# Kernel tuning notes

Hardware: AMD Instinct MI355X
Metric: run time of the kernel (lower is better)

## Reference

```python
import jax, jax.numpy as jnp
import numpy as np

IMG_H = 448
IMG_W = 448
NEG = jnp.float32(-1e30)


def make_anchors(h, w, stride, size):
    # centers at (x*stride, y*stride), single scale, ratio 1; row-major (y, x) order
    ys = jnp.arange(h, dtype=jnp.float32) * stride
    xs = jnp.arange(w, dtype=jnp.float32) * stride
    cy, cx = jnp.meshgrid(ys, xs, indexing='ij')
    cx, cy = cx.reshape(-1), cy.reshape(-1)
    half = 0.5 * size
    return jnp.stack([cx - half, cy - half, cx + half, cy + half], axis=1)  # [h*w, 4]


def iou_one_vs_all(box, boxes):
    x1 = jnp.maximum(box[0], boxes[:, 0]); y1 = jnp.maximum(box[1], boxes[:, 1])
    x2 = jnp.minimum(box[2], boxes[:, 2]); y2 = jnp.minimum(box[3], boxes[:, 3])
    inter = jnp.maximum(x2 - x1, 0.) * jnp.maximum(y2 - y1, 0.)
    a1 = (box[2] - box[0]) * (box[3] - box[1])
    a2 = (boxes[:, 2] - boxes[:, 0]) * (boxes[:, 3] - boxes[:, 1])
    return inter / (a1 + a2 - inter)


def nms_topk(anchors, scores, valid, iou_thr, topk):
    # greedy NMS: invalid (<= mean) boxes get -inf score so they are never selected
    s0 = jnp.where(valid, scores, NEG)

    def body(k, carry):
        s, out = carry
        idx = jnp.argmax(s)
        box = anchors[idx]
        sup = iou_one_vs_all(box, anchors) > iou_thr
        s = jnp.where(sup, NEG, s).at[idx].set(NEG)
        out = out.at[k].set(box)
        return (s, out)

    _, out = jax.lax.fori_loop(0, topk, body, (s0, jnp.zeros((topk, 4), jnp.float32)))
    return out  # [topk, 4]


def get_att_roi(att, stride, size, iou_thr, topk):
    n, _, h, w = att.shape
    corner = jnp.zeros((h, w), att.dtype).at[int(0.1 * h):int(0.9 * h), int(0.1 * w):int(0.9 * w)].set(1.0)
    scores = (att[:, 0] * corner).reshape(n, -1)
    valid = scores > scores.mean(axis=1, keepdims=True)  # score threshold = per-sample mean
    anchors = make_anchors(h, w, float(stride), float(size))
    boxes = jax.vmap(lambda s, v: nms_topk(anchors, s, v, iou_thr, topk))(scores, valid)  # [n, topk, 4]
    boxes = jnp.stack([
        jnp.maximum(boxes[..., 0], 0.),
        jnp.maximum(boxes[..., 1], 0.),
        jnp.minimum(boxes[..., 2], IMG_W - 1.),
        jnp.minimum(boxes[..., 3], IMG_H - 1.),
    ], axis=-1)
    ids = jnp.broadcast_to(jnp.arange(n, dtype=jnp.float32)[:, None, None], (n, topk, 1))
    return jnp.concatenate([ids, boxes], axis=-1).reshape(n * topk, 5)


def crop_resize(xi, x1i, y1i, cw, ch):
    # bilinear resize of integer crop xi[:, y1i:y1i+ch, x1i:x1i+cw] to full (H, W),
    # align_corners=False (matches F.interpolate)
    C, H, W = xi.shape

    def axis_idx(n_out, start, clen):
        s = jnp.maximum((jnp.arange(n_out, dtype=jnp.float32) + 0.5) * (clen.astype(jnp.float32) / n_out) - 0.5, 0.)
        i0 = jnp.floor(s).astype(jnp.int32)
        i1 = jnp.minimum(i0 + 1, clen - 1)
        return start + i0, start + i1, s - i0

    gy0, gy1, fy = axis_idx(H, y1i, ch)
    gx0, gx1, fx = axis_idx(W, x1i, cw)
    x00 = xi[:, gy0[:, None], gx0[None, :]]
    x01 = xi[:, gy0[:, None], gx1[None, :]]
    x10 = xi[:, gy1[:, None], gx0[None, :]]
    x11 = xi[:, gy1[:, None], gx1[None, :]]
    top = x00 + fx[None, None, :] * (x01 - x00)
    bot = x10 + fx[None, None, :] * (x11 - x10)
    return top + fy[None, :, None] * (bot - top)


def forward(x2, x3, x4, x5):
    m3 = x3.mean(1, keepdims=True)
    m4 = x4.mean(1, keepdims=True)
    m5 = x5.mean(1, keepdims=True)
    roi3 = jax.lax.stop_gradient(get_att_roi(m3, 2 ** 3, 64, 0.05, 5))
    roi4 = jax.lax.stop_gradient(get_att_roi(m4, 2 ** 4, 128, 0.05, 3))
    roi5 = jax.lax.stop_gradient(get_att_roi(m5, 2 ** 5, 256, 0.05, 1))
    n = x2.shape[0]
    scale = float(2 ** 3)
    all_b = jnp.concatenate([
        roi3.reshape(n, 5, 5)[..., 1:],
        roi4.reshape(n, 3, 5)[..., 1:],
        roi5.reshape(n, 1, 5)[..., 1:],
    ], axis=1) / scale  # [n, 9, 4] in x2 feature coords
    x1i = jnp.floor(all_b[..., 0].min(1)).astype(jnp.int32)
    y1i = jnp.floor(all_b[..., 1].min(1)).astype(jnp.int32)
    x2i = jnp.floor(all_b[..., 2].max(1)).astype(jnp.int32)
    y2i = jnp.floor(all_b[..., 3].max(1)).astype(jnp.int32)
    crop = jax.vmap(crop_resize)(x2, x1i, y1i, x2i - x1i, y2i - y1i)
    return roi3, roi4, roi5, crop


def setup_inputs() -> dict:
    key = jax.random.key(0)
    k2, k3, k4, k5 = jax.random.split(key, 4)
    return {
        'x2': jax.random.normal(k2, (32, 256, 56, 56), jnp.float32),
        'x3': jax.random.normal(k3, (32, 256, 56, 56), jnp.float32),
        'x4': jax.random.normal(k4, (32, 256, 28, 28), jnp.float32),
        'x5': jax.random.normal(k5, (32, 256, 14, 14), jnp.float32),
    }


def reference(x2, x3, x4, x5):
    return forward(x2, x3, x4, x5)
```

## Files before the change

kernel.cpp:

```cpp
#include <hip/hip_runtime.h>

#define NEGV (-1e30f)

template <int H, int W, int R0, int R1>
__device__ __forceinline__ void mean_body(int blk, const float* __restrict__ x,
                                          float* __restrict__ scores,
                                          float4* part) {
    constexpr int HW = H * W;
    constexpr int QUADS = HW / 4;
    const int tid = threadIdx.x;
    const int cg = tid >> 5;
    const int pl = tid & 31;
    const int q = blk * 32 + pl;

    const int b = q / QUADS;
    const int quad = q - b * QUADS;
    const float* base = x + (size_t)b * 256 * HW + (size_t)cg * 32 * HW + quad * 4;

    float4 acc = make_float4(0.f, 0.f, 0.f, 0.f);
#pragma unroll 8
    for (int c = 0; c < 32; ++c) {
        const float4 v = *reinterpret_cast<const float4*>(base + (size_t)c * HW);
        acc.x += v.x; acc.y += v.y; acc.z += v.z; acc.w += v.w;
    }
    part[tid] = acc;
    __syncthreads();

    if (tid < 32) {
        float4 s = part[pl];
#pragma unroll
        for (int g = 1; g < 8; ++g) {
            const float4 v = part[g * 32 + pl];
            s.x += v.x; s.y += v.y; s.z += v.z; s.w += v.w;
        }
        const int p0 = quad * 4;
        float r[4] = {s.x, s.y, s.z, s.w};
        float o[4];
#pragma unroll
        for (int e = 0; e < 4; ++e) {
            const int p = p0 + e;
            const int y = p / W;
            const int xx = p - y * W;
            const float val = r[e] * (1.0f / 256.0f);
            const bool in = (y >= R0) && (y < R1) && (xx >= R0) && (xx < R1);
            o[e] = in ? val : 0.0f;
        }
        *reinterpret_cast<float4*>(scores + (size_t)b * HW + p0) =
            make_float4(o[0], o[1], o[2], o[3]);
    }
}

__global__ __launch_bounds__(256) void mean_all_kernel(const float* __restrict__ x3,
                                                       const float* __restrict__ x4,
                                                       const float* __restrict__ x5,
                                                       float* __restrict__ sc3,
                                                       float* __restrict__ sc4,
                                                       float* __restrict__ sc5) {
    __shared__ float4 part[256];
    const int bid = blockIdx.x;
    if (bid < 784) {
        mean_body<56, 56, 5, 50>(bid, x3, sc3, part);
    } else if (bid < 980) {
        mean_body<28, 28, 2, 25>(bid - 784, x4, sc4, part);
    } else {
        mean_body<14, 14, 1, 12>(bid - 980, x5, sc5, part);
    }
}

template <int HW, int W, int TOPK, int ISTRIDE, int ISIZE, int BOXOFF>
__device__ __forceinline__ void nms_wave(int b, const float* __restrict__ sc,
                                         float* __restrict__ obox,
                                         float (*sbox)[4]) {
    constexpr int NPT = (HW + 63) / 64;
    const int lane = threadIdx.x & 63;

    float s[NPT];
    float sum = 0.f;
#pragma unroll
    for (int i = 0; i < NPT; ++i) {
        const int j = lane + 64 * i;
        const float v = (j < HW) ? sc[j] : NEGV;
        s[i] = v;
        if (j < HW) sum += v;
    }
#pragma unroll
    for (int off = 32; off > 0; off >>= 1) sum += __shfl_down(sum, off, 64);
    const float mean = __shfl(sum, 0, 64) / (float)HW;

#pragma unroll
    for (int i = 0; i < NPT; ++i) s[i] = (s[i] > mean) ? s[i] : NEGV;

    constexpr float half = 0.5f * (float)ISIZE;
    constexpr float area2 = 2.0f * (float)ISIZE * (float)ISIZE;

    for (int k = 0; k < TOPK; ++k) {
        float bv = -3.0e38f;
        int bi = 0x7fffffff;
#pragma unroll
        for (int i = 0; i < NPT; ++i) {
            if (s[i] > bv) { bv = s[i]; bi = lane + 64 * i; }
        }
#pragma unroll
        for (int off = 32; off > 0; off >>= 1) {
            const float ov = __shfl_down(bv, off, 64);
            const int oi = __shfl_down(bi, off, 64);
            if (ov > bv || (ov == bv && oi < bi)) { bv = ov; bi = oi; }
        }
        const int wi = __shfl(bi, 0, 64);

        const int gy = wi / W;
        const int gx = wi - gy * W;
        const float bx1 = (float)gx * (float)ISTRIDE - half;
        const float by1 = (float)gy * (float)ISTRIDE - half;
        const float bx2 = (float)gx * (float)ISTRIDE + half;
        const float by2 = (float)gy * (float)ISTRIDE + half;

        if (lane == 0) {
            const float c0 = fmaxf(bx1, 0.f);
            const float c1 = fmaxf(by1, 0.f);
            const float c2 = fminf(bx2, 447.f);
            const float c3 = fminf(by2, 447.f);
            float* r = obox + k * 5;
            r[0] = (float)b;
            r[1] = c0; r[2] = c1; r[3] = c2; r[4] = c3;
            sbox[BOXOFF + k][0] = c0;
            sbox[BOXOFF + k][1] = c1;
            sbox[BOXOFF + k][2] = c2;
            sbox[BOXOFF + k][3] = c3;
        }

#pragma unroll
        for (int i = 0; i < NPT; ++i) {
            const int j = lane + 64 * i;
            const int ay = j / W;
            const int ax = j - ay * W;
            const float acx = (float)ax * (float)ISTRIDE;
            const float acy = (float)ay * (float)ISTRIDE;
            const float ix1 = fmaxf(bx1, acx - half);
            const float iy1 = fmaxf(by1, acy - half);
            const float ix2 = fminf(bx2, acx + half);
            const float iy2 = fminf(by2, acy + half);
            const float inter = fmaxf(ix2 - ix1, 0.f) * fmaxf(iy2 - iy1, 0.f);
            const float iou = inter / (area2 - inter);
            if (iou > 0.05f || j == wi) s[i] = NEGV;
        }
    }
}

__global__ __launch_bounds__(256) void nms_tables_kernel(const float* __restrict__ sc3,
                                                         const float* __restrict__ sc4,
                                                         const float* __restrict__ sc5,
                                                         float* __restrict__ out,
                                                         int* __restrict__ ty0, int* __restrict__ ty1,
                                                         float* __restrict__ tfy,
                                                         int* __restrict__ tx0, int* __restrict__ tx1,
                                                         float* __restrict__ tfx,
                                                         int* __restrict__ bnds) {
    __shared__ float sbox[9][4];
    __shared__ int sb[4];

    const int b = blockIdx.x;
    const int tid = threadIdx.x;
    const int wave = tid >> 6;

    if (wave == 0) {
        nms_wave<3136, 56, 5, 8, 64, 0>(b, sc3 + (size_t)b * 3136, out + (size_t)b * 25, sbox);
    } else if (wave == 1) {
        nms_wave<784, 28, 3, 16, 128, 5>(b, sc4 + (size_t)b * 784, out + 800 + (size_t)b * 15, sbox);
    } else if (wave == 2) {
        nms_wave<196, 14, 1, 32, 256, 8>(b, sc5 + (size_t)b * 196, out + 1280 + (size_t)b * 5, sbox);
    }
    __syncthreads();

    if (tid == 0) {
        float x1 = 3.0e38f, y1 = 3.0e38f, x2 = -3.0e38f, y2 = -3.0e38f;
#pragma unroll
        for (int i = 0; i < 9; ++i) {
            x1 = fminf(x1, sbox[i][0]);
            y1 = fminf(y1, sbox[i][1]);
            x2 = fmaxf(x2, sbox[i][2]);
            y2 = fmaxf(y2, sbox[i][3]);
        }
        const int x1i = (int)floorf(x1 * 0.125f);
        const int y1i = (int)floorf(y1 * 0.125f);
        const int x2i = (int)floorf(x2 * 0.125f);
        const int y2i = (int)floorf(y2 * 0.125f);
        sb[0] = x1i; sb[1] = y1i; sb[2] = x2i - x1i; sb[3] = y2i - y1i;
        bnds[b * 2 + 0] = y1i;
        bnds[b * 2 + 1] = y2i - y1i;
    }
    __syncthreads();

    if (tid < 112) {
        const int axis = tid / 56;
        const int o = tid - axis * 56;
        if (axis == 0) {
            const int ch = sb[3];
            const float s = fmaxf(((float)o + 0.5f) * ((float)ch / 56.0f) - 0.5f, 0.f);
            const int i0 = (int)s;
            const int i1 = min(i0 + 1, ch - 1);
            ty0[b * 56 + o] = i0 * 56;
            ty1[b * 56 + o] = i1 * 56;
            tfy[b * 56 + o] = s - (float)i0;
        } else {
            const int cw = sb[2];
            const int x1i = sb[0];
            const float s = fmaxf(((float)o + 0.5f) * ((float)cw / 56.0f) - 0.5f, 0.f);
            const int i0 = (int)s;
            const int i1 = min(i0 + 1, cw - 1);
            tx0[b * 56 + o] = x1i + i0;
            tx1[b * 56 + o] = x1i + i1;
            tfx[b * 56 + o] = s - (float)i0;
        }
    }
}

__global__ __launch_bounds__(448) void crop_kernel(const float* __restrict__ x2,
                                                   const int* __restrict__ bnds,
                                                   const int* __restrict__ ty0,
                                                   const int* __restrict__ ty1,
                                                   const float* __restrict__ tfy,
                                                   const int* __restrict__ tx0,
                                                   const int* __restrict__ tx1,
                                                   const float* __restrict__ tfx,
                                                   float* __restrict__ outc) {
    __shared__ float sp[3136];
    __shared__ int sy0[56], sy1[56];
    __shared__ float sfy[56];
    __shared__ int sx0[56], sx1[56];
    __shared__ float sfx[56];

    const int bc = blockIdx.x;
    const int b = bc >> 8;
    const int tid = threadIdx.x;

    const int y1i = bnds[b * 2 + 0];
    const int ch = bnds[b * 2 + 1];

    if (tid < 336) {
        const int a = tid / 56;
        const int o = tid - a * 56;
        const int gi = b * 56 + o;
        switch (a) {
            case 0: sy0[o] = ty0[gi]; break;
            case 1: sy1[o] = ty1[gi]; break;
            case 2: sfy[o] = tfy[gi]; break;
            case 3: sx0[o] = tx0[gi]; break;
            case 4: sx1[o] = tx1[gi]; break;
            default: sfx[o] = tfx[gi]; break;
        }
    }

    const float4* src4 = reinterpret_cast<const float4*>(x2 + (size_t)bc * 3136 + y1i * 56);
    float4* sp4 = reinterpret_cast<float4*>(sp);
    const int n4 = ch * 14;
    for (int i = tid; i < n4; i += 448) sp4[i] = src4[i];
    __syncthreads();

    const int y0 = tid / 56;
    const int xx = tid - y0 * 56;
    const int gx0 = sx0[xx];
    const int gx1 = sx1[xx];
    const float fx = sfx[xx];

    float* op = outc + (size_t)bc * 3136;

#pragma unroll
    for (int i = 0; i < 7; ++i) {
        const int y = y0 + 8 * i;
        const int r0 = sy0[y];
        const int r1 = sy1[y];
        const float fy = sfy[y];
        const float v00 = sp[r0 + gx0];
        const float v01 = sp[r0 + gx1];
        const float v10 = sp[r1 + gx0];
        const float v11 = sp[r1 + gx1];
        const float top = v00 + fx * (v01 - v00);
        const float bot = v10 + fx * (v11 - v10);
        op[tid + 448 * i] = top + fy * (bot - top);
    }
}

extern "C" void kernel_launch(void* const* d_in, const int* in_sizes, int n_in,
                              void* d_out, int out_size, void* d_ws, size_t ws_size,
                              hipStream_t stream) {
    const float* x2 = (const float*)d_in[0];
    const float* x3 = (const float*)d_in[1];
    const float* x4 = (const float*)d_in[2];
    const float* x5 = (const float*)d_in[3];
    float* out = (float*)d_out;

    float* sc3 = (float*)d_ws;
    float* sc4 = sc3 + 32 * 3136;
    float* sc5 = sc4 + 32 * 784;
    int* ty0 = (int*)(sc5 + 32 * 196);
    int* ty1 = ty0 + 32 * 56;
    int* tx0 = ty1 + 32 * 56;
    int* tx1 = tx0 + 32 * 56;
    float* tfy = (float*)(tx1 + 32 * 56);
    float* tfx = tfy + 32 * 56;
    int* bnds = (int*)(tfx + 32 * 56);

    mean_all_kernel<<<1029, 256, 0, stream>>>(x3, x4, x5, sc3, sc4, sc5);
    nms_tables_kernel<<<32, 256, 0, stream>>>(sc3, sc4, sc5, out,
                                              ty0, ty1, tfy, tx0, tx1, tfx, bnds);
    crop_kernel<<<8192, 448, 0, stream>>>(x2, bnds, ty0, ty1, tfy, tx0, tx1, tfx,
                                          out + 1440);
}
```

Before: 304.0 us.

## Compute interpolation tables in crop kernel and read source planes directly

The interpolation index and weight tables move out of the NMS kernel and are rebuilt in shared memory by each crop block from four bounds integers. The crop kernel no longer stages the cropped rows into shared memory; it gathers bilinear samples straight from global memory. Each block now covers four channel planes instead of one, so there are a quarter as many blocks and the table setup is shared across planes. This removes the table round-trip through global memory and the staging copy, but relies on cache hits for the repeated, scattered global reads.

```diff
diff --git a/kernel.cpp b/kernel.cpp
--- a/kernel.cpp
+++ b/kernel.cpp
@@ -147,17 +147,12 @@
     }
 }
 
-__global__ __launch_bounds__(256) void nms_tables_kernel(const float* __restrict__ sc3,
+__global__ __launch_bounds__(256) void nms_bounds_kernel(const float* __restrict__ sc3,
                                                          const float* __restrict__ sc4,
                                                          const float* __restrict__ sc5,
                                                          float* __restrict__ out,
-                                                         int* __restrict__ ty0, int* __restrict__ ty1,
-                                                         float* __restrict__ tfy,
-                                                         int* __restrict__ tx0, int* __restrict__ tx1,
-                                                         float* __restrict__ tfx,
                                                          int* __restrict__ bnds) {
     __shared__ float sbox[9][4];
-    __shared__ int sb[4];
 
     const int b = blockIdx.x;
     const int tid = threadIdx.x;
@@ -185,76 +180,50 @@
         const int y1i = (int)floorf(y1 * 0.125f);
         const int x2i = (int)floorf(x2 * 0.125f);
         const int y2i = (int)floorf(y2 * 0.125f);
-        sb[0] = x1i; sb[1] = y1i; sb[2] = x2i - x1i; sb[3] = y2i - y1i;
-        bnds[b * 2 + 0] = y1i;
-        bnds[b * 2 + 1] = y2i - y1i;
-    }
-    __syncthreads();
+        bnds[b * 4 + 0] = x1i;
+        bnds[b * 4 + 1] = y1i;
+        bnds[b * 4 + 2] = x2i - x1i;
+        bnds[b * 4 + 3] = y2i - y1i;
+    }
+}
+
+__global__ __launch_bounds__(448) void crop_kernel(const float* __restrict__ x2,
+                                                   const int* __restrict__ bnds,
+                                                   float* __restrict__ outc) {
+    __shared__ int sy0[56], sy1[56];
+    __shared__ float sfy[56];
+    __shared__ int sx0[56], sx1[56];
+    __shared__ float sfx[56];
+
+    const int blk = blockIdx.x;
+    const int b = blk >> 6;
+    const int c0 = (blk & 63) * 4;
+    const int tid = threadIdx.x;
+
+    const int x1i = bnds[b * 4 + 0];
+    const int y1i = bnds[b * 4 + 1];
+    const int cw = bnds[b * 4 + 2];
+    const int ch = bnds[b * 4 + 3];
 
     if (tid < 112) {
         const int axis = tid / 56;
         const int o = tid - axis * 56;
         if (axis == 0) {
-            const int ch = sb[3];
             const float s = fmaxf(((float)o + 0.5f) * ((float)ch / 56.0f) - 0.5f, 0.f);
             const int i0 = (int)s;
             const int i1 = min(i0 + 1, ch - 1);
-            ty0[b * 56 + o] = i0 * 56;
-            ty1[b * 56 + o] = i1 * 56;
-            tfy[b * 56 + o] = s - (float)i0;
+            sy0[o] = (y1i + i0) * 56;
+            sy1[o] = (y1i + i1) * 56;
+            sfy[o] = s - (float)i0;
         } else {
-            const int cw = sb[2];
-            const int x1i = sb[0];
             const float s = fmaxf(((float)o + 0.5f) * ((float)cw / 56.0f) - 0.5f, 0.f);
             const int i0 = (int)s;
             const int i1 = min(i0 + 1, cw - 1);
-            tx0[b * 56 + o] = x1i + i0;
-            tx1[b * 56 + o] = x1i + i1;
-            tfx[b * 56 + o] = s - (float)i0;
-        }
-    }
-}
-
-__global__ __launch_bounds__(448) void crop_kernel(const float* __restrict__ x2,
-                                                   const int* __restrict__ bnds,
-                                                   const int* __restrict__ ty0,
-                                                   const int* __restrict__ ty1,
-                                                   const float* __restrict__ tfy,
-                                                   const int* __restrict__ tx0,
-                                                   const int* __restrict__ tx1,
-                                                   const float* __restrict__ tfx,
-                                                   float* __restrict__ outc) {
-    __shared__ float sp[3136];
-    __shared__ int sy0[56], sy1[56];
-    __shared__ float sfy[56];
-    __shared__ int sx0[56], sx1[56];
-    __shared__ float sfx[56];
-
-    const int bc = blockIdx.x;
-    const int b = bc >> 8;
-    const int tid = threadIdx.x;
-
-    const int y1i = bnds[b * 2 + 0];
-    const int ch = bnds[b * 2 + 1];
-
-    if (tid < 336) {
-        const int a = tid / 56;
-        const int o = tid - a * 56;
-        const int gi = b * 56 + o;
-        switch (a) {
-            case 0: sy0[o] = ty0[gi]; break;
-            case 1: sy1[o] = ty1[gi]; break;
-            case 2: sfy[o] = tfy[gi]; break;
-            case 3: sx0[o] = tx0[gi]; break;
-            case 4: sx1[o] = tx1[gi]; break;
-            default: sfx[o] = tfx[gi]; break;
-        }
-    }
-
-    const float4* src4 = reinterpret_cast<const float4*>(x2 + (size_t)bc * 3136 + y1i * 56);
-    float4* sp4 = reinterpret_cast<float4*>(sp);
-    const int n4 = ch * 14;
-    for (int i = tid; i < n4; i += 448) sp4[i] = src4[i];
+            sx0[o] = x1i + i0;
+            sx1[o] = x1i + i1;
+            sfx[o] = s - (float)i0;
+        }
+    }
     __syncthreads();
 
     const int y0 = tid / 56;
@@ -263,21 +232,24 @@
     const int gx1 = sx1[xx];
     const float fx = sfx[xx];
 
-    float* op = outc + (size_t)bc * 3136;
-
-#pragma unroll
-    for (int i = 0; i < 7; ++i) {
-        const int y = y0 + 8 * i;
-        const int r0 = sy0[y];
-        const int r1 = sy1[y];
-        const float fy = sfy[y];
-        const float v00 = sp[r0 + gx0];
-        const float v01 = sp[r0 + gx1];
-        const float v10 = sp[r1 + gx0];
-        const float v11 = sp[r1 + gx1];
-        const float top = v00 + fx * (v01 - v00);
-        const float bot = v10 + fx * (v11 - v10);
-        op[tid + 448 * i] = top + fy * (bot - top);
+    const size_t base = (size_t)(b * 256 + c0) * 3136;
+    for (int p = 0; p < 4; ++p) {
+        const float* plane = x2 + base + (size_t)p * 3136;
+        float* op = outc + base + (size_t)p * 3136;
+#pragma unroll
+        for (int i = 0; i < 7; ++i) {
+            const int y = y0 + 8 * i;
+            const int r0 = sy0[y];
+            const int r1 = sy1[y];
+            const float fy = sfy[y];
+            const float v00 = plane[r0 + gx0];
+            const float v01 = plane[r0 + gx1];
+            const float v10 = plane[r1 + gx0];
+            const float v11 = plane[r1 + gx1];
+            const float top = v00 + fx * (v01 - v00);
+            const float bot = v10 + fx * (v11 - v10);
+            op[tid + 448 * i] = top + fy * (bot - top);
+        }
     }
 }
 
@@ -293,17 +265,9 @@
     float* sc3 = (float*)d_ws;
     float* sc4 = sc3 + 32 * 3136;
     float* sc5 = sc4 + 32 * 784;
-    int* ty0 = (int*)(sc5 + 32 * 196);
-    int* ty1 = ty0 + 32 * 56;
-    int* tx0 = ty1 + 32 * 56;
-    int* tx1 = tx0 + 32 * 56;
-    float* tfy = (float*)(tx1 + 32 * 56);
-    float* tfx = tfy + 32 * 56;
-    int* bnds = (int*)(tfx + 32 * 56);
+    int* bnds = (int*)(sc5 + 32 * 196);
 
     mean_all_kernel<<<1029, 256, 0, stream>>>(x3, x4, x5, sc3, sc4, sc5);
-    nms_tables_kernel<<<32, 256, 0, stream>>>(sc3, sc4, sc5, out,
-                                              ty0, ty1, tfy, tx0, tx1, tfx, bnds);
-    crop_kernel<<<8192, 448, 0, stream>>>(x2, bnds, ty0, ty1, tfy, tx0, tx1, tfx,
-                                          out + 1440);
-}
+    nms_bounds_kernel<<<32, 256, 0, stream>>>(sc3, sc4, sc5, out, bnds);
+    crop_kernel<<<2048, 448, 0, stream>>>(x2, bnds, out + 1440);
+}
```

Result: slower. 313.4 us (+3.1%).
